# Optimization experiments

Measured on AMD Instinct MI355X. Metric: run time of the kernel, lower is better.

Reference implementation:

```python
import jax, jax.numpy as jnp
import numpy as np

B, IN, H = 8192, 1024, 1024
WRANK, UR0, UR1, G = 256, 64, 32, 2
HG = H // G


def setup_inputs() -> dict:
    key = jax.random.key(0)
    ks = jax.random.split(key, 24)
    r = lambda k, shp: 0.1 * jax.random.normal(k, shp, dtype=jnp.float32)
    inp = {
        "x": jax.random.normal(ks[0], (B, IN), dtype=jnp.float32),
        "h": jax.random.normal(ks[1], (B, H), dtype=jnp.float32),
        "c": jax.random.normal(ks[2], (B, H), dtype=jnp.float32),
        "W": r(ks[3], (IN, WRANK)),
        "W1": r(ks[4], (WRANK, H)),
        "W2": r(ks[5], (WRANK, H)),
        "W3": r(ks[6], (WRANK, H)),
        "W4": r(ks[7], (WRANK, H)),
        "U": r(ks[8], (G, HG, UR0)),
        "U1": r(ks[9], (G, UR0, HG)),
        "U2": r(ks[10], (G, UR0, HG)),
        "U3": r(ks[11], (G, UR0, HG)),
        "U4": r(ks[12], (G, UR0, HG)),
        "UU": r(ks[13], (G, HG, UR1)),
        "UU1": r(ks[14], (G, UR1, HG)),
        "UU2": r(ks[15], (G, UR1, HG)),
        "UU3": r(ks[16], (G, UR1, HG)),
        "UU4": r(ks[17], (G, UR1, HG)),
        "bias_f": jnp.ones((1, H), dtype=jnp.float32),
        "bias_i": jnp.ones((1, H), dtype=jnp.float32),
        "bias_c": jnp.ones((1, H), dtype=jnp.float32),
        "bias_o": jnp.ones((1, H), dtype=jnp.float32),
    }
    return inp


def _grouped(hg, Ushare, Ui):
    # hg: [B, g, hg]; Ushare: [g, hg, r]; Ui: [g, r, hg] -> [B, H]
    t = jnp.einsum('bgd,gdr->bgr', hg, Ushare)
    return jnp.einsum('bgr,grd->bgd', t, Ui).reshape(hg.shape[0], H)


def reference(x, h, c, W, W1, W2, W3, W4, U, U1, U2, U3, U4,
              UU, UU1, UU2, UU3, UU4, bias_f, bias_i, bias_c, bias_o):
    # low-rank W path
    xw = x @ W                      # [B, wRank]
    wVal1, wVal2, wVal3, wVal4 = xw @ W1, xw @ W2, xw @ W3, xw @ W4

    # grouped low-rank U path (diagonal groups)
    hg = h.reshape(B, G, HG)
    tU = jnp.einsum('bgd,gdr->bgr', hg, U)          # shared projection
    uVal1 = jnp.einsum('bgr,grd->bgd', tU, U1).reshape(B, H)
    uVal2 = jnp.einsum('bgr,grd->bgd', tU, U2).reshape(B, H)
    uVal3 = jnp.einsum('bgr,grd->bgd', tU, U3).reshape(B, H)
    uVal4 = jnp.einsum('bgr,grd->bgd', tU, U4).reshape(B, H)

    # grouped UU path on group-rotated h (index = [1..g-1, 0])
    hg3 = jnp.roll(hg, -1, axis=1)
    tUU = jnp.einsum('bgd,gdr->bgr', hg3, UU)
    uuVal1 = jnp.einsum('bgr,grd->bgd', tUU, UU1).reshape(B, H)
    uuVal2 = jnp.einsum('bgr,grd->bgd', tUU, UU2).reshape(B, H)
    uuVal3 = jnp.einsum('bgr,grd->bgd', tUU, UU3).reshape(B, H)
    uuVal4 = jnp.einsum('bgr,grd->bgd', tUU, UU4).reshape(B, H)

    matVal_i = wVal1 + uVal1 + uuVal1
    matVal_f = wVal2 + uVal2 + uuVal2
    matVal_o = wVal3 + uVal3 + uuVal3
    matVal_c = wVal4 + uVal4 + uuVal4

    i = jax.nn.sigmoid(matVal_i + bias_i)
    f = jax.nn.sigmoid(matVal_f + bias_f)
    o = jax.nn.sigmoid(matVal_o + bias_o)
    c_tilda = jnp.tanh(matVal_c + bias_c)

    c_next = f * c + i * c_tilda
    h_next = o * jnp.tanh(c_next)
    return (c_next, h_next)
```

## Files before the change

kernel.cpp:

```cpp
#include <hip/hip_runtime.h>
#include <hip/hip_bf16.h>

#define B_ROWS 8192
#define IN_DIM 1024
#define H_DIM  1024
#define WRANK  256
#define UR0    64
#define UR1    32
#define HGD    512
#define KTOT   384
#define A2_LD  512

typedef __attribute__((ext_vector_type(8))) short bf16x8;
typedef __attribute__((ext_vector_type(4))) float f32x4;
typedef __attribute__((ext_vector_type(4))) float float4v;

__device__ __forceinline__ unsigned short f2bf(float f) {
    union { float f; unsigned u; } v; v.f = f;
    unsigned r = v.u + 0x7FFF + ((v.u >> 16) & 1);
    return (unsigned short)(r >> 16);
}

__device__ __forceinline__ void gld16(void* lds, const void* g) {
    __builtin_amdgcn_global_load_lds(
        (const __attribute__((address_space(1))) unsigned int*)g,
        (__attribute__((address_space(3))) unsigned int*)lds, 16, 0, 0);
}

__device__ __forceinline__ float fsig(float x)  { return 1.f / (1.f + __expf(-x)); }
__device__ __forceinline__ float ftanh(float x) { return 1.f - 2.f / (__expf(2.f * x) + 1.f); }

__global__ __launch_bounds__(256)
void pack_weights(const float* __restrict__ W,
                  const float* __restrict__ W1, const float* __restrict__ W2,
                  const float* __restrict__ W3, const float* __restrict__ W4,
                  const float* __restrict__ U,  const float* __restrict__ U1,
                  const float* __restrict__ U2, const float* __restrict__ U3,
                  const float* __restrict__ U4,
                  const float* __restrict__ UU, const float* __restrict__ UU1,
                  const float* __restrict__ UU2,const float* __restrict__ UU3,
                  const float* __restrict__ UU4,
                  unsigned short* __restrict__ WbfT,
                  unsigned short* __restrict__ HPbf,
                  unsigned short* __restrict__ GateBT)
{
    const float* Wg[4]  = {W1, W2, W3, W4};
    const float* Ug[4]  = {U1, U2, U3, U4};
    const float* UUg[4] = {UU1, UU2, UU3, UU4};
    const long N_WT = 256L * 1024;
    const long N_HP = 256L * 512;
    const long N_GB = 4L * 1024 * KTOT;
    const long total = N_WT + N_HP + N_GB;
    for (long t = blockIdx.x * 256L + threadIdx.x; t < total; t += (long)gridDim.x * 256L) {
        if (t < N_WT) {
            int n = (int)(t >> 10), p = (int)(t & 1023);
            int span = p >> 6, slp = (p >> 3) & 7, e = p & 7;
            int k = span * 64 + ((slp ^ (n & 7)) << 3) + e;
            WbfT[t] = f2bf(W[(size_t)k * WRANK + n]);
        } else if (t < N_WT + N_HP) {
            long u = t - N_WT;
            int n = (int)(u >> 9), p = (int)(u & 511);
            int span = p >> 6, slp = (p >> 3) & 7, e = p & 7;
            int k = span * 64 + ((slp ^ (n & 7)) << 3) + e;
            float v;
            if (n < 64)       v = U [(size_t)k * UR0 + n];
            else if (n < 96)  v = UU[(size_t)(HGD + k) * UR1 + (n - 64)];
            else if (n < 128) v = 0.f;
            else if (n < 192) v = U [(size_t)(HGD + k) * UR0 + (n - 128)];
            else if (n < 224) v = UU[(size_t)k * UR1 + (n - 192)];
            else              v = 0.f;
            HPbf[u] = f2bf(v);
        } else {
            long u = t - N_WT - N_HP;
            int q = (int)(u / (1024L * KTOT));
            long w = u - (long)q * 1024 * KTOT;
            int n = (int)(w / KTOT), p = (int)(w % KTOT);
            int span = p >> 6, slp = (p >> 3) & 7, e = p & 7;
            int k = span * 64 + ((slp ^ (n & 7)) << 3) + e;
            int g = n >> 9, nn = n & 511;
            float v;
            if (k < WRANK)            v = Wg[q][(size_t)k * H_DIM + n];
            else if (k < WRANK + UR0) v = Ug[q][((size_t)g * UR0 + (k - WRANK)) * HGD + nn];
            else if (k < 352)         v = UUg[q][((size_t)g * UR1 + (k - 320)) * HGD + nn];
            else                      v = 0.f;
            GateBT[u] = f2bf(v);
        }
    }
}

__global__ __launch_bounds__(256, 2)
void s1_kernel(const float* __restrict__ x, const float* __restrict__ h,
               const unsigned short* __restrict__ WbfT,
               const unsigned short* __restrict__ HPbf,
               unsigned short* __restrict__ A2)
{
    __shared__ short As[128 * 64];
    __shared__ short Bs[64 * 64];

    const int flat = blockIdx.x;
    const int id = (flat & 7) * 64 + (flat >> 3);
    const int bx = id & 7, by = id >> 3;
    const int m0 = by * 128;

    const bool pa = bx < 4;
    const int Kdim = pa ? IN_DIM : HGD;
    const float* Af = pa ? x : h;
    const int a_off = pa ? 0 : ((bx - 4) >> 1) * HGD;
    const unsigned short* Bw = pa ? (WbfT + (size_t)(bx * 64) * IN_DIM)
                                  : (HPbf + (size_t)((bx - 4) * 64) * HGD);
    const int ldbw = pa ? IN_DIM : HGD;
    const int ccol0 = pa ? bx * 64 : WRANK + (bx - 4) * 64;

    const int tid = threadIdx.x, lane = tid & 63, wid = tid >> 6;
    const int wr = wid >> 1, wc = wid & 1;
    const int lr = lane & 15, lh = lane >> 4;

    f32x4 acc[4][2];
    #pragma unroll
    for (int i = 0; i < 4; ++i)
        #pragma unroll
        for (int j = 0; j < 2; ++j) acc[i][j] = (f32x4){0.f, 0.f, 0.f, 0.f};

    for (int k0 = 0; k0 < Kdim; k0 += 64) {
        #pragma unroll
        for (int t = 0; t < 2; ++t) {
            int u = wid + t * 4;
            const char* src = (const char*)Bw
                + ((size_t)(u * 8 + (lane >> 3)) * ldbw + k0) * 2 + (lane & 7) * 16;
            gld16((char*)Bs + u * 1024, src);
        }
        #pragma unroll
        for (int t = 0; t < 4; ++t) {
            int c = tid + t * 256;
            int row = c >> 3, slot = c & 7;
            const float* p = Af + (size_t)(m0 + row) * 1024 + a_off + k0 + slot * 8;
            float4v f0 = *(const float4v*)p, f1 = *(const float4v*)(p + 4);
            union { bf16x8 v; unsigned short s[8]; } uv;
            uv.s[0] = f2bf(f0.x); uv.s[1] = f2bf(f0.y);
            uv.s[2] = f2bf(f0.z); uv.s[3] = f2bf(f0.w);
            uv.s[4] = f2bf(f1.x); uv.s[5] = f2bf(f1.y);
            uv.s[6] = f2bf(f1.z); uv.s[7] = f2bf(f1.w);
            *(bf16x8*)((char*)As + row * 128 + ((slot ^ (row & 7)) << 4)) = uv.v;
        }
        __syncthreads();
        #pragma unroll
        for (int ks = 0; ks < 2; ++ks) {
            bf16x8 af[4];
            #pragma unroll
            for (int i = 0; i < 4; ++i) {
                int r = wr * 64 + i * 16 + lr;
                af[i] = *(const bf16x8*)((const char*)As + r * 128 + (((ks * 4 + lh) ^ (r & 7)) << 4));
            }
            #pragma unroll
            for (int j = 0; j < 2; ++j) {
                int r = wc * 32 + j * 16 + lr;
                bf16x8 rb = *(const bf16x8*)((const char*)Bs + r * 128 + (((ks * 4 + lh) ^ (r & 7)) << 4));
                #pragma unroll
                for (int i = 0; i < 4; ++i)
                    acc[i][j] = __builtin_amdgcn_mfma_f32_16x16x32_bf16(af[i], rb, acc[i][j], 0, 0, 0);
            }
        }
        __syncthreads();
    }

    #pragma unroll
    for (int i = 0; i < 4; ++i) {
        #pragma unroll
        for (int j = 0; j < 2; ++j) {
            int ncol = ccol0 + wc * 32 + j * 16 + lr;
            int span = ncol >> 6, sl = (ncol >> 3) & 7, e = ncol & 7;
            #pragma unroll
            for (int rr = 0; rr < 4; ++rr) {
                int brow = m0 + wr * 64 + i * 16 + lh * 4 + rr;
                int phys = span * 64 + ((sl ^ (brow & 7)) << 3) + e;
                A2[(size_t)brow * A2_LD + phys] = f2bf(acc[i][j][rr]);
            }
        }
    }
}

__global__ __launch_bounds__(256, 2)
void s2_kernel(const unsigned short* __restrict__ A2,
               const unsigned short* __restrict__ GateBT,
               const float* __restrict__ bias_f, const float* __restrict__ bias_i,
               const float* __restrict__ bias_c, const float* __restrict__ bias_o,
               const float* __restrict__ cin,
               float* __restrict__ cout, float* __restrict__ hout)
{
    __shared__ short As[128 * 64];
    __shared__ short Bs[4][64 * 64];

    const int flat = blockIdx.x;
    const int id = (flat & 7) * 128 + (flat >> 3);
    const int nt = id & 15, mt = id >> 4;
    const int m0 = mt * 128, n0 = nt * 64, g = n0 >> 9;

    const int tid = threadIdx.x, lane = tid & 63, wid = tid >> 6;
    const int wr = wid >> 1, wc = wid & 1;
    const int lr = lane & 15, lh = lane >> 4;

    f32x4 acc[4][4][2];
    #pragma unroll
    for (int q = 0; q < 4; ++q)
        #pragma unroll
        for (int i = 0; i < 4; ++i)
            #pragma unroll
            for (int j = 0; j < 2; ++j) acc[q][i][j] = (f32x4){0.f, 0.f, 0.f, 0.f};

    for (int s = 0; s < 6; ++s) {
        const int ms = (s < 4) ? s : ((s == 4) ? 4 + 2 * g : 5 + 2 * (g ^ 1));
        #pragma unroll
        for (int t = 0; t < 4; ++t) {
            int u = wid * 4 + t;
            const char* src = (const char*)A2
                + (size_t)(m0 + u * 8 + (lane >> 3)) * (A2_LD * 2) + ms * 128 + (lane & 7) * 16;
            gld16((char*)As + u * 1024, src);
        }
        #pragma unroll
        for (int t = 0; t < 8; ++t) {
            int q = t >> 1;
            int u = (t & 1) * 4 + wid;
            const char* src = (const char*)GateBT
                + (size_t)(q * 1024 + n0 + u * 8 + (lane >> 3)) * (KTOT * 2) + s * 128 + (lane & 7) * 16;
            gld16((char*)Bs[q] + u * 1024, src);
        }
        __syncthreads();
        #pragma unroll
        for (int ks = 0; ks < 2; ++ks) {
            bf16x8 af[4];
            #pragma unroll
            for (int i = 0; i < 4; ++i) {
                int r = wr * 64 + i * 16 + lr;
                af[i] = *(const bf16x8*)((const char*)As + r * 128 + (((ks * 4 + lh) ^ (r & 7)) << 4));
            }
            #pragma unroll
            for (int q = 0; q < 4; ++q) {
                #pragma unroll
                for (int j = 0; j < 2; ++j) {
                    int r = wc * 32 + j * 16 + lr;
                    bf16x8 rb = *(const bf16x8*)((const char*)Bs[q] + r * 128 + (((ks * 4 + lh) ^ (r & 7)) << 4));
                    #pragma unroll
                    for (int i = 0; i < 4; ++i)
                        acc[q][i][j] = __builtin_amdgcn_mfma_f32_16x16x32_bf16(af[i], rb, acc[q][i][j], 0, 0, 0);
                }
            }
        }
        __syncthreads();
    }

    #pragma unroll
    for (int j = 0; j < 2; ++j) {
        int ncol = n0 + wc * 32 + j * 16 + lr;
        float Bi = bias_i[ncol], Bf = bias_f[ncol];
        float Bo = bias_o[ncol], Bc = bias_c[ncol];
        #pragma unroll
        for (int i = 0; i < 4; ++i) {
            #pragma unroll
            for (int rr = 0; rr < 4; ++rr) {
                int brow = m0 + wr * 64 + i * 16 + lh * 4 + rr;
                float mi = acc[0][i][j][rr] + Bi;
                float mf = acc[1][i][j][rr] + Bf;
                float mo = acc[2][i][j][rr] + Bo;
                float mc = acc[3][i][j][rr] + Bc;
                float iv = fsig(mi), fv = fsig(mf), ov = fsig(mo);
                float ct = ftanh(mc);
                float cv = cin[(size_t)brow * H_DIM + ncol];
                float cn = fv * cv + iv * ct;
                float hn = ov * ftanh(cn);
                cout[(size_t)brow * H_DIM + ncol] = cn;
                hout[(size_t)brow * H_DIM + ncol] = hn;
            }
        }
    }
}

extern "C" void kernel_launch(void* const* d_in, const int* in_sizes, int n_in,
                              void* d_out, int out_size, void* d_ws, size_t ws_size,
                              hipStream_t stream)
{
    const float* x   = (const float*)d_in[0];
    const float* h   = (const float*)d_in[1];
    const float* c   = (const float*)d_in[2];
    const float* W   = (const float*)d_in[3];
    const float* W1  = (const float*)d_in[4];
    const float* W2  = (const float*)d_in[5];
    const float* W3  = (const float*)d_in[6];
    const float* W4  = (const float*)d_in[7];
    const float* U   = (const float*)d_in[8];
    const float* U1  = (const float*)d_in[9];
    const float* U2  = (const float*)d_in[10];
    const float* U3  = (const float*)d_in[11];
    const float* U4  = (const float*)d_in[12];
    const float* UU  = (const float*)d_in[13];
    const float* UU1 = (const float*)d_in[14];
    const float* UU2 = (const float*)d_in[15];
    const float* UU3 = (const float*)d_in[16];
    const float* UU4 = (const float*)d_in[17];
    const float* bias_f = (const float*)d_in[18];
    const float* bias_i = (const float*)d_in[19];
    const float* bias_c = (const float*)d_in[20];
    const float* bias_o = (const float*)d_in[21];

    unsigned short* A2     = (unsigned short*)d_ws;
    unsigned short* WbfT   = A2   + (size_t)B_ROWS * A2_LD;
    unsigned short* HPbf   = WbfT + 256L * 1024;
    unsigned short* GateBT = HPbf + 256L * 512;

    float* c_out = (float*)d_out;
    float* h_out = c_out + (size_t)B_ROWS * H_DIM;

    pack_weights<<<dim3(2048), dim3(256), 0, stream>>>(
        W, W1, W2, W3, W4, U, U1, U2, U3, U4, UU, UU1, UU2, UU3, UU4,
        WbfT, HPbf, GateBT);

    s1_kernel<<<dim3(512), dim3(256), 0, stream>>>(x, h, WbfT, HPbf, A2);

    s2_kernel<<<dim3(1024), dim3(256), 0, stream>>>(
        A2, GateBT, bias_f, bias_i, bias_c, bias_o, c, c_out, h_out);
}
```

Measured before the change: 97.30 us.

## Double-buffer s2 GEMM LDS tiles with 512-thread blocks over 256-row tiles

The s2 kernel now uses 512-thread blocks covering 256 rows per block, with double-buffered LDS for the A and gate-weight tiles. The next K-slice is prefetched while MFMAs run on the current one, using explicit vmcnt waits and raw barriers. MFMA sections also run at raised wave priority. Together these aim to hide global-load latency and share each gate-weight tile across more rows, at the cost of more LDS per block (about 96KB), which may reduce occupancy below the declared two blocks per CU.

Measured after the change: 94.00 us. -3.4%, faster.

```diff
diff --git a/kernel.cpp b/kernel.cpp
--- a/kernel.cpp
+++ b/kernel.cpp
@@ -179,7 +179,7 @@
     }
 }
 
-__global__ __launch_bounds__(256, 2)
+__global__ __launch_bounds__(512, 2)
 void s2_kernel(const unsigned short* __restrict__ A2,
                const unsigned short* __restrict__ GateBT,
                const float* __restrict__ bias_f, const float* __restrict__ bias_i,
@@ -187,17 +187,18 @@
                const float* __restrict__ cin,
                float* __restrict__ cout, float* __restrict__ hout)
 {
-    __shared__ short As[128 * 64];
-    __shared__ short Bs[4][64 * 64];
+    __shared__ short As[2][256 * 64];
+    __shared__ short Bs[2][4][64 * 64];
 
     const int flat = blockIdx.x;
-    const int id = (flat & 7) * 128 + (flat >> 3);
+    const int id = (flat & 7) * 64 + (flat >> 3);
     const int nt = id & 15, mt = id >> 4;
-    const int m0 = mt * 128, n0 = nt * 64, g = n0 >> 9;
+    const int m0 = mt * 256, n0 = nt * 64, g = n0 >> 9;
 
     const int tid = threadIdx.x, lane = tid & 63, wid = tid >> 6;
     const int wr = wid >> 1, wc = wid & 1;
     const int lr = lane & 15, lh = lane >> 4;
+    const int l8 = lane >> 3, l7 = lane & 7;
 
     f32x4 acc[4][4][2];
     #pragma unroll
@@ -207,46 +208,66 @@
             #pragma unroll
             for (int j = 0; j < 2; ++j) acc[q][i][j] = (f32x4){0.f, 0.f, 0.f, 0.f};
 
+#define STAGE_S2(buf, s) do {                                                        \
+    const int _ms = ((s) < 4) ? (s) : (((s) == 4) ? 4 + 2 * g : 5 + 2 * (g ^ 1));    \
+    _Pragma("unroll")                                                                \
+    for (int t = 0; t < 4; ++t) {                                                    \
+        int u = wid * 4 + t;                                                         \
+        gld16((char*)&As[buf][0] + u * 1024,                                         \
+              (const char*)A2 + ((size_t)(m0 + u * 8 + l8) * A2_LD + _ms * 64) * 2   \
+              + l7 * 16);                                                            \
+    }                                                                                \
+    _Pragma("unroll")                                                                \
+    for (int t = 0; t < 4; ++t) {                                                    \
+        int v = wid * 4 + t, q = v >> 3, uu = v & 7;                                 \
+        gld16((char*)&Bs[buf][q][0] + uu * 1024,                                     \
+              (const char*)GateBT + ((size_t)(q * 1024 + n0 + uu * 8 + l8) * KTOT    \
+              + (s) * 64) * 2 + l7 * 16);                                            \
+    } } while (0)
+
+    STAGE_S2(0, 0);
+
+    #pragma unroll
     for (int s = 0; s < 6; ++s) {
-        const int ms = (s < 4) ? s : ((s == 4) ? 4 + 2 * g : 5 + 2 * (g ^ 1));
-        #pragma unroll
-        for (int t = 0; t < 4; ++t) {
-            int u = wid * 4 + t;
-            const char* src = (const char*)A2
-                + (size_t)(m0 + u * 8 + (lane >> 3)) * (A2_LD * 2) + ms * 128 + (lane & 7) * 16;
-            gld16((char*)As + u * 1024, src);
-        }
-        #pragma unroll
-        for (int t = 0; t < 8; ++t) {
-            int q = t >> 1;
-            int u = (t & 1) * 4 + wid;
-            const char* src = (const char*)GateBT
-                + (size_t)(q * 1024 + n0 + u * 8 + (lane >> 3)) * (KTOT * 2) + s * 128 + (lane & 7) * 16;
-            gld16((char*)Bs[q] + u * 1024, src);
-        }
-        __syncthreads();
+        const int cur = s & 1;
+        if (s < 5) {
+            STAGE_S2(cur ^ 1, s + 1);
+            asm volatile("s_waitcnt vmcnt(8)" ::: "memory");
+        } else {
+            asm volatile("s_waitcnt vmcnt(0)" ::: "memory");
+        }
+        __builtin_amdgcn_s_barrier();
+        asm volatile("" ::: "memory");
+        __builtin_amdgcn_s_setprio(1);
         #pragma unroll
         for (int ks = 0; ks < 2; ++ks) {
             bf16x8 af[4];
             #pragma unroll
             for (int i = 0; i < 4; ++i) {
                 int r = wr * 64 + i * 16 + lr;
-                af[i] = *(const bf16x8*)((const char*)As + r * 128 + (((ks * 4 + lh) ^ (r & 7)) << 4));
+                af[i] = *(const bf16x8*)((const char*)&As[cur][0] + r * 128
+                        + (((ks * 4 + lh) ^ (r & 7)) << 4));
             }
             #pragma unroll
             for (int q = 0; q < 4; ++q) {
                 #pragma unroll
                 for (int j = 0; j < 2; ++j) {
                     int r = wc * 32 + j * 16 + lr;
-                    bf16x8 rb = *(const bf16x8*)((const char*)Bs[q] + r * 128 + (((ks * 4 + lh) ^ (r & 7)) << 4));
+                    bf16x8 rb = *(const bf16x8*)((const char*)&Bs[cur][q][0] + r * 128
+                                + (((ks * 4 + lh) ^ (r & 7)) << 4));
                     #pragma unroll
                     for (int i = 0; i < 4; ++i)
-                        acc[q][i][j] = __builtin_amdgcn_mfma_f32_16x16x32_bf16(af[i], rb, acc[q][i][j], 0, 0, 0);
+                        acc[q][i][j] = __builtin_amdgcn_mfma_f32_16x16x32_bf16(
+                            af[i], rb, acc[q][i][j], 0, 0, 0);
                 }
             }
         }
-        __syncthreads();
-    }
+        __builtin_amdgcn_s_setprio(0);
+        asm volatile("" ::: "memory");
+        __builtin_amdgcn_s_barrier();
+        asm volatile("" ::: "memory");
+    }
+#undef STAGE_S2
 
     #pragma unroll
     for (int j = 0; j < 2; ++j) {
@@ -315,6 +336,6 @@
 
     s1_kernel<<<dim3(512), dim3(256), 0, stream>>>(x, h, WbfT, HPbf, A2);
 
-    s2_kernel<<<dim3(1024), dim3(256), 0, stream>>>(
+    s2_kernel<<<dim3(512), dim3(512), 0, stream>>>(
         A2, GateBT, bias_f, bias_i, bias_c, bias_o, c, c_out, h_out);
 }
```
